# Kernel tuning notes

Hardware: AMD Instinct MI355X
Metric: run time of the kernel (lower is better)

## Reference

```python
import jax, jax.numpy as jnp
import numpy as np

N = 50000      # nodes
E = 800000     # edges
C = 128        # in channels
H = 128        # hidden1 = hidden2 = hidden3
B = 256        # graphs in batch
CLS = 10       # classes
MLP_H = 64
EPS = 1e-5


def _lin_params(key, fan_in, fan_out):
    k1, k2 = jax.random.split(key)
    s = 1.0 / np.sqrt(fan_in)
    W = jax.random.uniform(k1, (fan_in, fan_out), jnp.float32, -s, s)
    b = jax.random.uniform(k2, (fan_out,), jnp.float32, -s, s)
    return W, b


def setup_inputs() -> dict:
    key = jax.random.key(0)
    ks = jax.random.split(key, 10)
    x = jax.random.normal(ks[0], (N, C), jnp.float32)
    edge_index = jax.random.randint(ks[1], (2, E), 0, N)
    edge_attr = jax.random.uniform(ks[2], (E,), jnp.float32)
    batch = jnp.sort(jax.random.randint(ks[3], (N,), 0, B))
    W1, b1 = _lin_params(ks[4], C, H)
    W2, b2 = _lin_params(ks[5], H, H)
    W3, b3 = _lin_params(ks[6], H, H)
    gamma = jnp.ones((H,), jnp.float32)
    beta = jnp.zeros((H,), jnp.float32)
    Wm1, bm1 = _lin_params(ks[7], H, MLP_H)
    Wm2, bm2 = _lin_params(ks[8], MLP_H, CLS)
    return dict(x=x, edge_index=edge_index, edge_attr=edge_attr, batch=batch,
                W1=W1, b1=b1, W2=W2, b2=b2, W3=W3, b3=b3,
                gamma=gamma, beta=beta, Wm1=Wm1, bm1=bm1, Wm2=Wm2, bm2=bm2)


def gcn_conv(x, src, dst, ew, W, b):
    # PyG GCNConv: linear (no bias) -> gcn_norm with self-loops -> scatter-add -> +bias
    h = x @ W                                                  # [N, out]
    deg = jax.ops.segment_sum(ew, dst, num_segments=N) + 1.0   # self-loop weight 1
    dinv = jnp.where(deg > 0, jax.lax.rsqrt(deg), 0.0)
    norm = dinv[src] * ew * dinv[dst]                          # [E]
    agg = jax.ops.segment_sum(norm[:, None] * h[src], dst, num_segments=N)
    agg = agg + h * (dinv * dinv)[:, None]                     # self-loop messages
    return agg + b


def reference(x, edge_index, edge_attr, batch,
              W1, b1, W2, b2, W3, b3, gamma, beta, Wm1, bm1, Wm2, bm2):
    src, dst = edge_index[0], edge_index[1]
    ew = edge_attr.reshape(-1)
    h = jax.nn.relu(gcn_conv(x, src, dst, ew, W1, b1))
    h = jax.nn.relu(gcn_conv(h, src, dst, ew, W2, b2))
    h = jax.nn.relu(gcn_conv(h, src, dst, ew, W3, b3))
    # BatchNorm (training-mode batch stats, biased variance)
    mu = jnp.mean(h, axis=0)
    var = jnp.mean((h - mu) ** 2, axis=0)
    h = (h - mu) * jax.lax.rsqrt(var + EPS) * gamma + beta
    # global_mean_pool over graph ids
    counts = jax.ops.segment_sum(jnp.ones((N,), jnp.float32), batch, num_segments=B)
    g = jax.ops.segment_sum(h, batch, num_segments=B) / jnp.maximum(counts, 1.0)[:, None]
    # MLP head (two stacked linears, no activation between)
    pred = (g @ Wm1 + bm1) @ Wm2 + bm2
    return pred
```

## Files before the change

kernel.cpp:

```cpp
#include <hip/hip_runtime.h>
#include <hip/hip_bf16.h>

#define NN 50000
#define EE 800000
#define HH 128
#define BB 256
#define CLS 10
#define MLPH 64
#define CAP 64

typedef __attribute__((ext_vector_type(8))) short short8;
typedef __attribute__((ext_vector_type(4))) float floatx4;

__device__ __forceinline__ float bflo(unsigned u){ unsigned v = u << 16; return __builtin_bit_cast(float, v); }
__device__ __forceinline__ float bfhi(unsigned u){ unsigned v = u & 0xffff0000u; return __builtin_bit_cast(float, v); }
__device__ __forceinline__ unsigned short f2bf(float f){
  unsigned u = __builtin_bit_cast(unsigned, f);
  u += 0x7fffu + ((u >> 16) & 1u);
  return (unsigned short)(u >> 16);
}
__device__ __forceinline__ unsigned pack2(float a, float b){
  return (unsigned)f2bf(a) | ((unsigned)f2bf(b) << 16);
}

__global__ __launch_bounds__(256) void init_k(int* cnt, float* bnsum, float* bnsqs){
  int i = blockIdx.x * 256 + threadIdx.x;
  if (i < NN) cnt[i] = 0;
  if (i < HH) { bnsum[i] = 0.0f; bnsqs[i] = 0.0f; }
}

__global__ __launch_bounds__(256) void scatter_k(const int* __restrict__ src, const int* __restrict__ dst,
                                                 const float* __restrict__ ew,
                                                 int* __restrict__ cnt, int2* __restrict__ ebuf){
  int e = blockIdx.x * 256 + threadIdx.x;
  if (e >= EE) return;
  int d = dst[e];
  int p = atomicAdd(&cnt[d], 1);
  if (p < CAP){
    int2 rec; rec.x = src[e]; rec.y = __builtin_bit_cast(int, ew[e]);
    ebuf[(size_t)d * CAP + p] = rec;
  }
}

__global__ __launch_bounds__(256) void degdinv_k(const int2* __restrict__ ebuf, const int* __restrict__ cnt,
                                                 float* __restrict__ dinv){
  int node = blockIdx.x * 4 + (threadIdx.x >> 6);
  if (node >= NN) return;
  int lane = threadIdx.x & 63;
  int c = min(cnt[node], CAP);
  float w = 0.0f;
  if (lane < c) w = __builtin_bit_cast(float, ebuf[(size_t)node * CAP + lane].y);
  #pragma unroll
  for (int off = 32; off; off >>= 1) w += __shfl_down(w, off);
  if (lane == 0) dinv[node] = rsqrtf(1.0f + w);
}

__global__ __launch_bounds__(256) void gbounds_k(const int* __restrict__ batch, int* gstart){
  int b = threadIdx.x;
  int lo = 0, hi = NN;
  while (lo < hi){
    int mid = (lo + hi) >> 1;
    if (batch[mid] < b) lo = mid + 1; else hi = mid;
  }
  gstart[b] = lo;
  if (b == 0) gstart[BB] = NN;
}

__global__ __launch_bounds__(256) void cvt_x_k(const float* __restrict__ x, unsigned* __restrict__ xb){
  int i = blockIdx.x * 256 + threadIdx.x;
  if (i >= NN * HH / 2) return;
  float2 v = ((const float2*)x)[i];
  xb[i] = pack2(v.x, v.y);
}

__global__ __launch_bounds__(256) void transpose3_k(const float* W1, const float* W2, const float* W3,
                                                    unsigned short* Wt1, unsigned short* Wt2, unsigned short* Wt3){
  int gi = blockIdx.x * 256 + threadIdx.x;
  int w = gi >> 14;
  int i = gi & 16383;
  const float* W = (w == 0) ? W1 : (w == 1) ? W2 : W3;
  unsigned short* Wt = (w == 0) ? Wt1 : (w == 1) ? Wt2 : Wt3;
  int n = i >> 7, k = i & 127;
  Wt[i] = f2bf(W[(k << 7) + n]);
}

__global__ __launch_bounds__(256) void gemm128_k(const unsigned short* __restrict__ X,
                                                 const unsigned short* __restrict__ Wt,
                                                 const float* __restrict__ dinv,
                                                 unsigned short* __restrict__ Gout, int nrows){
  __shared__ __align__(16) unsigned short lw[HH * 136];
  {
    const float4* s4 = (const float4*)Wt;
    float4* d4 = (float4*)lw;
    for (int i = threadIdx.x; i < 2048; i += 256){
      int row = i >> 4, off = i & 15;
      d4[row * 17 + off] = s4[i];
    }
  }
  __syncthreads();
  int wave = threadIdx.x >> 6;
  int lane = threadIdx.x & 63;
  int r16 = lane & 15, quad = lane >> 4;
  int m0 = blockIdx.x * 128 + wave * 32;

  short8 afrag[2][4];
  for (int rt = 0; rt < 2; ++rt){
    int m = m0 + rt * 16 + r16;
    int msafe = (m < nrows) ? m : 0;
    const short8* arow = (const short8*)(X + (size_t)msafe * HH);
    for (int kk = 0; kk < 4; ++kk) afrag[rt][kk] = arow[4 * kk + quad];
  }
  float dv0[4], dv1[4];
  for (int r = 0; r < 4; ++r){
    int m = m0 + quad * 4 + r;
    dv0[r] = (m < nrows) ? dinv[m] : 0.0f;
    int m2 = m0 + 16 + quad * 4 + r;
    dv1[r] = (m2 < nrows) ? dinv[m2] : 0.0f;
  }
  for (int ct = 0; ct < 8; ++ct){
    floatx4 acc0 = {0.f,0.f,0.f,0.f}, acc1 = {0.f,0.f,0.f,0.f};
    const short8* brow = (const short8*)(lw + (16 * ct + r16) * 136);
    for (int kk = 0; kk < 4; ++kk){
      short8 bfrag = brow[4 * kk + quad];
      acc0 = __builtin_amdgcn_mfma_f32_16x16x32_bf16(afrag[0][kk], bfrag, acc0, 0, 0, 0);
      acc1 = __builtin_amdgcn_mfma_f32_16x16x32_bf16(afrag[1][kk], bfrag, acc1, 0, 0, 0);
    }
    int c = 16 * ct + r16;
    for (int r = 0; r < 4; ++r){
      int m = m0 + quad * 4 + r;
      if (m < nrows) Gout[(size_t)m * HH + c] = f2bf(acc0[r] * dv0[r]);
      int m2 = m0 + 16 + quad * 4 + r;
      if (m2 < nrows) Gout[(size_t)m2 * HH + c] = f2bf(acc1[r] * dv1[r]);
    }
  }
}

__global__ __launch_bounds__(256) void aggregate_k(const unsigned short* __restrict__ Gin,
                                                   const int2* __restrict__ ebuf,
                                                   const int* __restrict__ cnt,
                                                   const float* __restrict__ dinv,
                                                   const float* __restrict__ bias,
                                                   unsigned short* __restrict__ Xout){
  int node = blockIdx.x * 4 + (threadIdx.x >> 6);
  if (node >= NN) return;
  int lane = threadIdx.x & 63;
  const unsigned* G = (const unsigned*)Gin;
  unsigned gs = G[(size_t)node * 64 + lane];
  float a0 = bflo(gs), a1 = bfhi(gs);
  int c = min(cnt[node], CAP);
  const int2* row = ebuf + (size_t)node * CAP;
  int j = 0;
  for (; j + 4 <= c; j += 4){
    int2 e0 = row[j], e1 = row[j+1], e2 = row[j+2], e3 = row[j+3];
    unsigned h0 = G[(size_t)e0.x * 64 + lane];
    unsigned h1 = G[(size_t)e1.x * 64 + lane];
    unsigned h2 = G[(size_t)e2.x * 64 + lane];
    unsigned h3 = G[(size_t)e3.x * 64 + lane];
    float w0 = __builtin_bit_cast(float, e0.y), w1 = __builtin_bit_cast(float, e1.y);
    float w2 = __builtin_bit_cast(float, e2.y), w3 = __builtin_bit_cast(float, e3.y);
    a0 = fmaf(w0, bflo(h0), a0); a1 = fmaf(w0, bfhi(h0), a1);
    a0 = fmaf(w1, bflo(h1), a0); a1 = fmaf(w1, bfhi(h1), a1);
    a0 = fmaf(w2, bflo(h2), a0); a1 = fmaf(w2, bfhi(h2), a1);
    a0 = fmaf(w3, bflo(h3), a0); a1 = fmaf(w3, bfhi(h3), a1);
  }
  for (; j < c; ++j){
    int2 e = row[j];
    unsigned hh = G[(size_t)e.x * 64 + lane];
    float w = __builtin_bit_cast(float, e.y);
    a0 = fmaf(w, bflo(hh), a0); a1 = fmaf(w, bfhi(hh), a1);
  }
  float di = dinv[node];
  float2 bb = ((const float2*)bias)[lane];
  a0 = fmaxf(fmaf(di, a0, bb.x), 0.0f);
  a1 = fmaxf(fmaf(di, a1, bb.y), 0.0f);
  ((unsigned*)Xout)[(size_t)node * 64 + lane] = pack2(a0, a1);
}

__global__ __launch_bounds__(256) void pool_k(const unsigned short* __restrict__ H3,
                                              const int* __restrict__ gstart,
                                              float* __restrict__ S, float* bnsum, float* bnsqs,
                                              float* cntf){
  __shared__ float rs0[256], rs1[256], rq0[256], rq1[256];
  int b = blockIdx.x;
  int t = threadIdx.x, colc = t & 63, sub = t >> 6;
  int start = gstart[b], end = gstart[b + 1];
  const unsigned* Hrow = (const unsigned*)H3;
  float s0 = 0, s1 = 0, q0 = 0, q1 = 0;
  #pragma unroll 4
  for (int n = start + sub; n < end; n += 4){
    unsigned h = Hrow[(size_t)n * 64 + colc];
    float a = bflo(h), c = bfhi(h);
    s0 += a; s1 += c; q0 += a * a; q1 += c * c;
  }
  rs0[t] = s0; rs1[t] = s1; rq0[t] = q0; rq1[t] = q1;
  __syncthreads();
  if (sub == 0){
    float t0 = rs0[colc] + rs0[colc + 64] + rs0[colc + 128] + rs0[colc + 192];
    float t1 = rs1[colc] + rs1[colc + 64] + rs1[colc + 128] + rs1[colc + 192];
    float u0 = rq0[colc] + rq0[colc + 64] + rq0[colc + 128] + rq0[colc + 192];
    float u1 = rq1[colc] + rq1[colc + 64] + rq1[colc + 128] + rq1[colc + 192];
    S[b * HH + 2 * colc]     = t0;
    S[b * HH + 2 * colc + 1] = t1;
    atomicAdd(&bnsum[2 * colc], t0);
    atomicAdd(&bnsum[2 * colc + 1], t1);
    atomicAdd(&bnsqs[2 * colc], u0);
    atomicAdd(&bnsqs[2 * colc + 1], u1);
    if (t == 0) cntf[b] = (float)(end - start);
  }
}

__global__ __launch_bounds__(64) void mlp_head_k(const float* __restrict__ S, const float* __restrict__ cntf,
                                                 const float* __restrict__ bnsum, const float* __restrict__ bnsqs,
                                                 const float* gamma, const float* beta,
                                                 const float* Wm1, const float* bm1,
                                                 const float* Wm2, const float* bm2,
                                                 float* out){
  __shared__ float gb[HH];
  __shared__ float t[MLPH];
  int b = blockIdx.x, j = threadIdx.x;
  float inv = 1.0f / fmaxf(cntf[b], 1.0f);
  for (int c = j; c < HH; c += 64){
    float mu = bnsum[c] * (1.0f / NN);
    float var = bnsqs[c] * (1.0f / NN) - mu * mu;
    float istd = rsqrtf(var + 1e-5f);
    float g = S[b * HH + c] * inv;
    gb[c] = (g - mu) * istd * gamma[c] + beta[c];
  }
  __syncthreads();
  float acc = bm1[j];
  for (int k = 0; k < HH; ++k) acc = fmaf(gb[k], Wm1[k * MLPH + j], acc);
  t[j] = acc;
  __syncthreads();
  if (j < CLS){
    float o = bm2[j];
    for (int k = 0; k < MLPH; ++k) o = fmaf(t[k], Wm2[k * CLS + j], o);
    out[b * CLS + j] = o;
  }
}

static inline size_t al(size_t x){ return (x + 255) & ~(size_t)255; }

extern "C" void kernel_launch(void* const* d_in, const int* in_sizes, int n_in,
                              void* d_out, int out_size, void* d_ws, size_t ws_size,
                              hipStream_t stream){
  const float* x     = (const float*)d_in[0];
  const int*   ei    = (const int*)d_in[1];
  const float* ea    = (const float*)d_in[2];
  const int*   batch = (const int*)d_in[3];
  const float* W1 = (const float*)d_in[4];
  const float* b1 = (const float*)d_in[5];
  const float* W2 = (const float*)d_in[6];
  const float* b2 = (const float*)d_in[7];
  const float* W3 = (const float*)d_in[8];
  const float* b3 = (const float*)d_in[9];
  const float* gamma = (const float*)d_in[10];
  const float* beta  = (const float*)d_in[11];
  const float* Wm1 = (const float*)d_in[12];
  const float* bm1 = (const float*)d_in[13];
  const float* Wm2 = (const float*)d_in[14];
  const float* bm2 = (const float*)d_in[15];
  const int* srcv = ei;
  const int* dstv = ei + EE;

  char* p = (char*)d_ws;
  float* dinv   = (float*)p;            p += al(NN * 4);
  int*   cnt    = (int*)p;              p += al(NN * 4);
  int*   gstart = (int*)p;              p += al((BB + 1) * 4);
  int2*  ebuf   = (int2*)p;             p += al((size_t)NN * CAP * 8);
  unsigned short* Wt1  = (unsigned short*)p; p += al(HH * HH * 2);
  unsigned short* Wt2  = (unsigned short*)p; p += al(HH * HH * 2);
  unsigned short* Wt3  = (unsigned short*)p; p += al(HH * HH * 2);
  unsigned short* bufA = (unsigned short*)p; p += al((size_t)NN * HH * 2);
  unsigned short* bufB = (unsigned short*)p; p += al((size_t)NN * HH * 2);
  float* S     = (float*)p;             p += al(BB * HH * 4);
  float* bnsum = (float*)p;             p += al(HH * 4);
  float* bnsqs = (float*)p;             p += al(HH * 4);
  float* cntf  = (float*)p;             p += al(BB * 4);

  const int nT = 256;
  dim3 gN((NN + 255) / 256), gE((EE + 255) / 256), gW((NN + 3) / 4);

  init_k<<<gN, nT, 0, stream>>>(cnt, bnsum, bnsqs);
  scatter_k<<<gE, nT, 0, stream>>>(srcv, dstv, ea, cnt, ebuf);
  degdinv_k<<<gW, nT, 0, stream>>>(ebuf, cnt, dinv);
  gbounds_k<<<dim3(1), nT, 0, stream>>>(batch, gstart);
  cvt_x_k<<<dim3((NN * HH / 2 + 255) / 256), nT, 0, stream>>>(x, (unsigned*)bufB);
  transpose3_k<<<dim3(192), nT, 0, stream>>>(W1, W2, W3, Wt1, Wt2, Wt3);

  dim3 gGemm((NN + 127) / 128);
  gemm128_k<<<gGemm, nT, 0, stream>>>(bufB, Wt1, dinv, bufA, NN);
  aggregate_k<<<gW, nT, 0, stream>>>(bufA, ebuf, cnt, dinv, b1, bufB);
  gemm128_k<<<gGemm, nT, 0, stream>>>(bufB, Wt2, dinv, bufA, NN);
  aggregate_k<<<gW, nT, 0, stream>>>(bufA, ebuf, cnt, dinv, b2, bufB);
  gemm128_k<<<gGemm, nT, 0, stream>>>(bufB, Wt3, dinv, bufA, NN);
  aggregate_k<<<gW, nT, 0, stream>>>(bufA, ebuf, cnt, dinv, b3, bufB);

  pool_k<<<dim3(BB), nT, 0, stream>>>(bufB, gstart, S, bnsum, bnsqs, cntf);
  mlp_head_k<<<dim3(BB), dim3(64), 0, stream>>>(S, cntf, bnsum, bnsqs, gamma, beta,
                                                Wm1, bm1, Wm2, bm2, (float*)d_out);
}
```

Baseline: 346.4 us.

## Vectorize GEMM output stores and split aggregate gather into four 16-byte sub-waves

The GEMM swaps its MFMA operands so each lane holds four consecutive channels of one row, which allows packed 8-byte stores in place of scalar 2-byte stores. The aggregate kernel loads a node's edge list once into lanes and broadcasts each entry with shuffles. It splits each wave into four groups that gather different neighbors with 16-byte loads, then reduces the partial sums through shared memory. This aims to raise memory-level parallelism and load width in the gather, at the cost of a block-wide barrier and an LDS reduction. The early return for node >= NN is removed; this is safe only because NN is a multiple of 4.

```diff
diff --git a/kernel.cpp b/kernel.cpp
--- a/kernel.cpp
+++ b/kernel.cpp
@@ -103,34 +103,35 @@
   int r16 = lane & 15, quad = lane >> 4;
   int m0 = blockIdx.x * 128 + wave * 32;
 
-  short8 afrag[2][4];
-  for (int rt = 0; rt < 2; ++rt){
-    int m = m0 + rt * 16 + r16;
+  short8 xfrag[2][4];
+  float dv[2];
+  for (int nt = 0; nt < 2; ++nt){
+    int m = m0 + nt * 16 + r16;
     int msafe = (m < nrows) ? m : 0;
-    const short8* arow = (const short8*)(X + (size_t)msafe * HH);
-    for (int kk = 0; kk < 4; ++kk) afrag[rt][kk] = arow[4 * kk + quad];
-  }
-  float dv0[4], dv1[4];
-  for (int r = 0; r < 4; ++r){
-    int m = m0 + quad * 4 + r;
-    dv0[r] = (m < nrows) ? dinv[m] : 0.0f;
-    int m2 = m0 + 16 + quad * 4 + r;
-    dv1[r] = (m2 < nrows) ? dinv[m2] : 0.0f;
+    const short8* xrow = (const short8*)(X + (size_t)msafe * HH);
+    for (int kk = 0; kk < 4; ++kk) xfrag[nt][kk] = xrow[4 * kk + quad];
+    dv[nt] = (m < nrows) ? dinv[m] : 0.0f;
   }
   for (int ct = 0; ct < 8; ++ct){
     floatx4 acc0 = {0.f,0.f,0.f,0.f}, acc1 = {0.f,0.f,0.f,0.f};
-    const short8* brow = (const short8*)(lw + (16 * ct + r16) * 136);
+    const short8* wrow = (const short8*)(lw + (16 * ct + r16) * 136);
     for (int kk = 0; kk < 4; ++kk){
-      short8 bfrag = brow[4 * kk + quad];
-      acc0 = __builtin_amdgcn_mfma_f32_16x16x32_bf16(afrag[0][kk], bfrag, acc0, 0, 0, 0);
-      acc1 = __builtin_amdgcn_mfma_f32_16x16x32_bf16(afrag[1][kk], bfrag, acc1, 0, 0, 0);
+      short8 wfrag = wrow[4 * kk + quad];
+      acc0 = __builtin_amdgcn_mfma_f32_16x16x32_bf16(wfrag, xfrag[0][kk], acc0, 0, 0, 0);
+      acc1 = __builtin_amdgcn_mfma_f32_16x16x32_bf16(wfrag, xfrag[1][kk], acc1, 0, 0, 0);
     }
-    int c = 16 * ct + r16;
-    for (int r = 0; r < 4; ++r){
-      int m = m0 + quad * 4 + r;
-      if (m < nrows) Gout[(size_t)m * HH + c] = f2bf(acc0[r] * dv0[r]);
-      int m2 = m0 + 16 + quad * 4 + r;
-      if (m2 < nrows) Gout[(size_t)m2 * HH + c] = f2bf(acc1[r] * dv1[r]);
+    int ch0 = ct * 16 + quad * 4;
+    int m = m0 + r16;
+    if (m < nrows){
+      uint2 pk; pk.x = pack2(acc0[0] * dv[0], acc0[1] * dv[0]);
+      pk.y = pack2(acc0[2] * dv[0], acc0[3] * dv[0]);
+      ((uint2*)Gout)[((size_t)m * HH + ch0) >> 2] = pk;
+    }
+    int m2 = m0 + 16 + r16;
+    if (m2 < nrows){
+      uint2 pk; pk.x = pack2(acc1[0] * dv[1], acc1[1] * dv[1]);
+      pk.y = pack2(acc1[2] * dv[1], acc1[3] * dv[1]);
+      ((uint2*)Gout)[((size_t)m2 * HH + ch0) >> 2] = pk;
     }
   }
 }
@@ -141,34 +142,39 @@
                                                    const float* __restrict__ dinv,
                                                    const float* __restrict__ bias,
                                                    unsigned short* __restrict__ Xout){
-  int node = blockIdx.x * 4 + (threadIdx.x >> 6);
-  if (node >= NN) return;
-  int lane = threadIdx.x & 63;
-  const unsigned* G = (const unsigned*)Gin;
-  unsigned gs = G[(size_t)node * 64 + lane];
-  float a0 = bflo(gs), a1 = bfhi(gs);
+  __shared__ float part[4][4][16][8];
+  int wv = threadIdx.x >> 6, lane = threadIdx.x & 63;
+  int node = blockIdx.x * 4 + wv;
+  int g = lane >> 4, l = lane & 15;
   int c = min(cnt[node], CAP);
-  const int2* row = ebuf + (size_t)node * CAP;
-  int j = 0;
-  for (; j + 4 <= c; j += 4){
-    int2 e0 = row[j], e1 = row[j+1], e2 = row[j+2], e3 = row[j+3];
-    unsigned h0 = G[(size_t)e0.x * 64 + lane];
-    unsigned h1 = G[(size_t)e1.x * 64 + lane];
-    unsigned h2 = G[(size_t)e2.x * 64 + lane];
-    unsigned h3 = G[(size_t)e3.x * 64 + lane];
-    float w0 = __builtin_bit_cast(float, e0.y), w1 = __builtin_bit_cast(float, e1.y);
-    float w2 = __builtin_bit_cast(float, e2.y), w3 = __builtin_bit_cast(float, e3.y);
-    a0 = fmaf(w0, bflo(h0), a0); a1 = fmaf(w0, bfhi(h0), a1);
-    a0 = fmaf(w1, bflo(h1), a0); a1 = fmaf(w1, bfhi(h1), a1);
-    a0 = fmaf(w2, bflo(h2), a0); a1 = fmaf(w2, bfhi(h2), a1);
-    a0 = fmaf(w3, bflo(h3), a0); a1 = fmaf(w3, bfhi(h3), a1);
-  }
-  for (; j < c; ++j){
-    int2 e = row[j];
-    unsigned hh = G[(size_t)e.x * 64 + lane];
-    float w = __builtin_bit_cast(float, e.y);
-    a0 = fmaf(w, bflo(hh), a0); a1 = fmaf(w, bfhi(hh), a1);
-  }
+  int2 rec; rec.x = 0; rec.y = 0;
+  if (lane < c) rec = ebuf[(size_t)node * CAP + lane];
+  float acc[8] = {0,0,0,0,0,0,0,0};
+  const uint4* G4 = (const uint4*)Gin;
+  int steps = (c + 3) >> 2;
+  for (int j = 0; j < steps; ++j){
+    int idx = 4 * j + g;
+    int sx = __shfl(rec.x, idx);
+    float w = __builtin_bit_cast(float, __shfl(rec.y, idx));
+    if (idx >= c){ sx = 0; w = 0.0f; }
+    uint4 q = G4[(size_t)sx * 16 + l];
+    acc[0] = fmaf(w, bflo(q.x), acc[0]);
+    acc[1] = fmaf(w, bfhi(q.x), acc[1]);
+    acc[2] = fmaf(w, bflo(q.y), acc[2]);
+    acc[3] = fmaf(w, bfhi(q.y), acc[3]);
+    acc[4] = fmaf(w, bflo(q.z), acc[4]);
+    acc[5] = fmaf(w, bfhi(q.z), acc[5]);
+    acc[6] = fmaf(w, bflo(q.w), acc[6]);
+    acc[7] = fmaf(w, bfhi(q.w), acc[7]);
+  }
+  #pragma unroll
+  for (int k = 0; k < 8; ++k) part[wv][g][l][k] = acc[k];
+  __syncthreads();
+  int l0 = lane >> 2, k0 = (lane & 3) * 2;
+  float a0 = part[wv][0][l0][k0]   + part[wv][1][l0][k0]   + part[wv][2][l0][k0]   + part[wv][3][l0][k0];
+  float a1 = part[wv][0][l0][k0+1] + part[wv][1][l0][k0+1] + part[wv][2][l0][k0+1] + part[wv][3][l0][k0+1];
+  unsigned gs = ((const unsigned*)Gin)[(size_t)node * 64 + lane];
+  a0 += bflo(gs); a1 += bfhi(gs);
   float di = dinv[node];
   float2 bb = ((const float2*)bias)[lane];
   a0 = fmaxf(fmaf(di, a0, bb.x), 0.0f);
```

Result: faster. 324.2 us (-6.4%).
